# Kernel tuning notes

Measured on AMD Instinct MI355X. Metric: run time of the kernel, lower is better.

The kernel has to match this reference:

```python
import jax, jax.numpy as jnp
import numpy as np

B, C, H, W = 64, 3, 224, 224
DEPTH = 2
NUM_OPS = 14

def _lin(m, lo, hi):
    return lo + m * (hi - lo)

def _clip255(x):
    return jnp.clip(x, 0.0, 255.0)

def _affine_sample(img, a, b, c, d, e, f):
    # img: [C,H,W]; inverse map (x_out,y_out)->(a*x+b*y+c, d*x+e*y+f); bilinear, zero fill.
    ch, h, w = img.shape
    ys, xs = jnp.meshgrid(jnp.arange(h, dtype=img.dtype), jnp.arange(w, dtype=img.dtype), indexing='ij')
    sx = a * xs + b * ys + c
    sy = d * xs + e * ys + f
    x0 = jnp.floor(sx); y0 = jnp.floor(sy)
    wx = sx - x0; wy = sy - y0
    def gather(yi, xi):
        valid = (xi >= 0) & (xi <= w - 1) & (yi >= 0) & (yi <= h - 1)
        v = img[:, jnp.clip(yi, 0, h - 1).astype(jnp.int32), jnp.clip(xi, 0, w - 1).astype(jnp.int32)]
        return jnp.where(valid[None], v, 0.0)
    v00 = gather(y0, x0); v01 = gather(y0, x0 + 1)
    v10 = gather(y0 + 1, x0); v11 = gather(y0 + 1, x0 + 1)
    top = v00 * (1 - wx) + v01 * wx
    bot = v10 * (1 - wx) + v11 * wx
    return top * (1 - wy) + bot * wy

def _gray(img):
    lum = jnp.array([0.299, 0.587, 0.114], img.dtype)
    return jnp.einsum('chw,c->hw', img, lum)

def shear_x(img, m):
    v = _lin(m, -0.3, 0.3)
    return _affine_sample(img, 1.0, v, 0.0, 0.0, 1.0, 0.0)

def shear_y(img, m):
    v = _lin(m, -0.3, 0.3)
    return _affine_sample(img, 1.0, 0.0, 0.0, v, 1.0, 0.0)

def translate_x(img, m):
    v = _lin(m, -0.45, 0.45) * img.shape[2]
    return _affine_sample(img, 1.0, 0.0, v, 0.0, 1.0, 0.0)

def translate_y(img, m):
    v = _lin(m, -0.45, 0.45) * img.shape[1]
    return _affine_sample(img, 1.0, 0.0, 0.0, 0.0, 1.0, v)

def rotate(img, m):
    rad = _lin(m, -30.0, 30.0) * np.pi / 180.0
    cx = (img.shape[2] - 1) * 0.5
    cy = (img.shape[1] - 1) * 0.5
    cs, sn = jnp.cos(rad), jnp.sin(rad)
    c = cx - cs * cx - sn * cy
    f = cy + sn * cx - cs * cy
    return _affine_sample(img, cs, sn, c, -sn, cs, f)

def brightness(img, m):
    return _clip255(img * _lin(m, 0.1, 1.9))

def color(img, m):
    g = _gray(img)[None]
    return _clip255(g + _lin(m, 0.1, 1.9) * (img - g))

def sharpness(img, m):
    k = jnp.array([[1., 1., 1.], [1., 5., 1.], [1., 1., 1.]], img.dtype) / 13.0
    ch = img.shape[0]
    kern = jnp.tile(k[None, None], (ch, 1, 1, 1))  # [C,1,3,3] depthwise
    blur = jax.lax.conv_general_dilated(img[None], kern, (1, 1), 'SAME', feature_group_count=ch)[0]
    out = _clip255(blur + _lin(m, 0.1, 1.9) * (img - blur))
    # PIL keeps the 1-px border unchanged
    out = out.at[:, 0, :].set(img[:, 0, :]).at[:, -1, :].set(img[:, -1, :])
    out = out.at[:, :, 0].set(img[:, :, 0]).at[:, :, -1].set(img[:, :, -1])
    return out

def contrast(img, m):
    mu = jnp.mean(_gray(img))
    return _clip255(mu + _lin(m, 0.1, 1.9) * (img - mu))

def solarize(img, m):
    thr = _lin(m, 0.0, 256.0)
    return jnp.where(img < thr, img, 255.0 - img)

def posterize(img, m):
    nbits = jnp.round(_lin(m, 0.0, 4.0))  # bits removed -> keep 8-nbits
    q = 2.0 ** nbits
    return jnp.floor(img / q) * q

def equalize(img, m):
    def eq_ch(chan):
        v = jnp.clip(jnp.round(chan), 0, 255).astype(jnp.int32)
        hist = jnp.zeros(256, jnp.int32).at[v.ravel()].add(1)
        step = (jnp.sum(hist) - hist[255]) // 255
        cum = jnp.concatenate([jnp.zeros(1, jnp.int32), jnp.cumsum(hist)[:-1]])
        lut = jnp.where(step > 0,
                        jnp.clip((cum + step // 2) // jnp.maximum(step, 1), 0, 255),
                        jnp.arange(256))
        return lut[v].astype(chan.dtype)
    return jax.vmap(eq_ch)(img)

def autocontrast(img, m):
    lo = jnp.min(img, axis=(1, 2), keepdims=True)
    hi = jnp.max(img, axis=(1, 2), keepdims=True)
    scale = 255.0 / jnp.maximum(hi - lo, 1e-6)
    return jnp.where(hi > lo, _clip255((img - lo) * scale), img)

def identity(img, m):
    return img

BRANCHES = [shear_x, shear_y, translate_x, translate_y, rotate, brightness, color,
            sharpness, contrast, solarize, posterize, equalize, autocontrast, identity]

def setup_inputs() -> dict:
    key = jax.random.key(0)
    k1, k2, k3, k4, k5 = jax.random.split(key, 5)
    x = jax.random.uniform(k1, (B, C, H, W), jnp.float32)          # [0,1]; module scales by 255
    ra_deform = jax.random.uniform(k2, (DEPTH, B), jnp.float32)    # magnitudes in [0,1]
    op_idx = jax.random.randint(k3, (DEPTH, B), 0, NUM_OPS, jnp.int32)
    p = jax.random.uniform(k4, (DEPTH, B), jnp.float32, 0.2, 0.8)  # p_min_t..p_max_t
    apply_mask = jax.random.uniform(k5, (DEPTH, B), jnp.float32) < p
    return {"x": x, "ra_deform": ra_deform, "op_idx": op_idx, "apply_mask": apply_mask}

def reference(x, ra_deform, op_idx, apply_mask):
    x = x * jnp.where(jnp.max(x) <= 1.0, 255.0, 1.0)
    x = x.astype(jnp.float32)
    def apply_one(img, j, m, ap):
        out = jax.lax.switch(j, BRANCHES, img, m)
        return jnp.where(ap, out, img)
    for i in range(DEPTH):  # small fixed depth
        x = jax.vmap(apply_one)(x, op_idx[i], ra_deform[i], apply_mask[i])
    return jnp.clip(x / 255.0, 0.0, 1.0)
```

## Files before the change

kernel.cpp:

```cpp
#include <hip/hip_runtime.h>

#define WID 224
#define HGT 224
#define HWp 50176
#define CHW 150528
#define NB  64
#define NSL 2048
#define SCH 1568
#define NT  9408
#define TPI 147
#define TPC 49

#define OFF_MAXB   0
#define OFF_HIST1  256
#define OFF_PSUM0  49408
#define OFF_PMIN0  51456
#define OFF_PMAX0  57600
#define OFF_PHIST0 63744
#define OFF_PSUM1  3209472
#define OFF_PMIN1  3218880
#define OFF_PMAX1  3228288
#define OFF_INTER  3237696

__device__ __forceinline__ float clip255(float v){ return fminf(fmaxf(v, 0.f), 255.f); }

__device__ __forceinline__ float blk_reduce(float v, float* red, int tid, int op){
    red[tid] = v; __syncthreads();
    for (int s = 128; s > 0; s >>= 1){
        if (tid < s){
            float a = red[tid], b = red[tid+s];
            red[tid] = (op==0) ? a+b : (op==1 ? fminf(a,b) : fmaxf(a,b));
        }
        __syncthreads();
    }
    float r = red[0]; __syncthreads();
    return r;
}

__device__ __forceinline__ float samp(const float* __restrict__ pl, float yi, float xi, float scl){
    if (xi < 0.f || xi > (float)(WID-1) || yi < 0.f || yi > (float)(HGT-1)) return 0.f;
    return pl[(int)yi * WID + (int)xi] * scl;
}

__device__ __forceinline__ void lut_from_hist(const int* shh, float* slut, int tid){
    int step = (HWp - shh[255]) / 255;
    int cum = 0;
    for (int k = 0; k < tid; k++) cum += shh[k];
    int l = (step > 0) ? min(max((cum + (step >> 1)) / step, 0), 255) : tid;
    slut[tid] = (float)l;
}

__device__ __forceinline__ void apply_body(const float* __restrict__ img,
                                           int c, int p,
                                           int j, int ap, float m, float scl,
                                           float mu, float lo, float hi,
                                           const float* lut,
                                           float o[4])
{
    int y = p / WID;
    int x = p - y*WID;
    const float* pl = img + c*HWp;
    float4 v4 = *(const float4*)(pl + p);
    float iv[4] = {v4.x*scl, v4.y*scl, v4.z*scl, v4.w*scl};

    if (!ap) {
        #pragma unroll
        for (int k = 0; k < 4; k++) o[k] = iv[k];
        return;
    }
    switch (j){
    case 0: case 1: case 2: case 3: case 4: {
        float a = 1.f, bb = 0.f, cc = 0.f, dd = 0.f, ee = 1.f, ff = 0.f;
        if (j == 0)      bb = -0.3f + 0.6f*m;
        else if (j == 1) dd = -0.3f + 0.6f*m;
        else if (j == 2) cc = (-0.45f + 0.9f*m) * (float)WID;
        else if (j == 3) ff = (-0.45f + 0.9f*m) * (float)HGT;
        else {
            float deg = -30.f + 60.f*m;
            float rad = deg * (float)(3.14159265358979323846/180.0);
            float cs = cosf(rad), sn = sinf(rad);
            float cx = (WID-1)*0.5f, cy = (HGT-1)*0.5f;
            a = cs; bb = sn; dd = -sn; ee = cs;
            cc = cx - cs*cx - sn*cy;
            ff = cy + sn*cx - cs*cy;
        }
        float yf = (float)y;
        #pragma unroll
        for (int k = 0; k < 4; k++){
            float xf = (float)(x + k);
            float sx = a*xf + bb*yf + cc;
            float sy = dd*xf + ee*yf + ff;
            float x0f = floorf(sx), y0f = floorf(sy);
            float wx = sx - x0f, wy = sy - y0f;
            float v00 = samp(pl, y0f,     x0f,     scl);
            float v01 = samp(pl, y0f,     x0f+1.f, scl);
            float v10 = samp(pl, y0f+1.f, x0f,     scl);
            float v11 = samp(pl, y0f+1.f, x0f+1.f, scl);
            float top = v00*(1.f-wx) + v01*wx;
            float bot = v10*(1.f-wx) + v11*wx;
            o[k] = top*(1.f-wy) + bot*wy;
        }
        break; }
    case 5: {
        float f = 0.1f + 1.8f*m;
        #pragma unroll
        for (int k = 0; k < 4; k++) o[k] = clip255(iv[k]*f);
        break; }
    case 6: {
        float4 r4 = *(const float4*)(img + p);
        float4 g4 = *(const float4*)(img + HWp + p);
        float4 b4 = *(const float4*)(img + 2*HWp + p);
        float rr[4] = {r4.x*scl, r4.y*scl, r4.z*scl, r4.w*scl};
        float gg[4] = {g4.x*scl, g4.y*scl, g4.z*scl, g4.w*scl};
        float bl[4] = {b4.x*scl, b4.y*scl, b4.z*scl, b4.w*scl};
        float f = 0.1f + 1.8f*m;
        #pragma unroll
        for (int k = 0; k < 4; k++){
            float g = 0.299f*rr[k] + 0.587f*gg[k] + 0.114f*bl[k];
            o[k] = clip255(g + f*(iv[k] - g));
        }
        break; }
    case 7: {
        float f = 0.1f + 1.8f*m;
        #pragma unroll
        for (int k = 0; k < 4; k++){
            int xx = x + k;
            if (y == 0 || y == HGT-1 || xx == 0 || xx == WID-1) o[k] = iv[k];
            else {
                int q = p + k;
                float s8 = pl[q-WID-1] + pl[q-WID] + pl[q-WID+1]
                         + pl[q-1]     + pl[q+1]
                         + pl[q+WID-1] + pl[q+WID] + pl[q+WID+1];
                float blur = (s8*scl + 5.f*iv[k]) * (1.f/13.f);
                o[k] = clip255(blur + f*(iv[k] - blur));
            }
        }
        break; }
    case 8: {
        float f = 0.1f + 1.8f*m;
        #pragma unroll
        for (int k = 0; k < 4; k++) o[k] = clip255(mu + f*(iv[k] - mu));
        break; }
    case 9: {
        float thr = 256.f*m;
        #pragma unroll
        for (int k = 0; k < 4; k++) o[k] = (iv[k] < thr) ? iv[k] : 255.f - iv[k];
        break; }
    case 10: {
        float q = exp2f(rintf(4.f*m));
        #pragma unroll
        for (int k = 0; k < 4; k++) o[k] = floorf(iv[k]/q)*q;
        break; }
    case 11: {
        #pragma unroll
        for (int k = 0; k < 4; k++){
            int ivi = min(max((int)rintf(iv[k]), 0), 255);
            o[k] = lut[ivi];
        }
        break; }
    case 12: {
        float sc = 255.f / fmaxf(hi - lo, 1e-6f);
        #pragma unroll
        for (int k = 0; k < 4; k++)
            o[k] = (hi > lo) ? clip255((iv[k] - lo) * sc) : iv[k];
        break; }
    default:
        #pragma unroll
        for (int k = 0; k < 4; k++) o[k] = iv[k];
        break;
    }
}

__global__ void k1_stats(const float* __restrict__ x, const int* __restrict__ op,
                         const int* __restrict__ mask, float* __restrict__ wsf)
{
    __shared__ float red[256];
    __shared__ int sh[1536];
    int* ints = (int*)wsf;
    float* psum0 = wsf + OFF_PSUM0;
    float* pmin0 = wsf + OFF_PMIN0;
    float* pmax0 = wsf + OFF_PMAX0;
    int* phist0 = (int*)wsf + OFF_PHIST0;
    int* hist1  = (int*)wsf + OFF_HIST1;

    int blk = blockIdx.x, tid = threadIdx.x;
    if (tid < 24) hist1[blk*24 + tid] = 0;

    int b = blk >> 5, s = blk & 31;
    int j = op[b], ap = mask[b];
    bool needSum  = ap && (j == 8);
    bool needMM   = ap && (j == 12);
    bool needHist = ap && (j == 11);
    const float* img = x + (size_t)b * CHW;
    int p0 = s * SCH;
    const float GW[3] = {0.299f, 0.587f, 0.114f};

    float mx = 0.f, gs = 0.f;
    for (int c = 0; c < 3; c++){
        const float* pl = img + c*HWp + p0;
        float lo = 3.4e38f, hi = 0.f, cs = 0.f;
        for (int p = tid*4; p < SCH; p += 1024){
            float4 v = *(const float4*)(pl + p);
            float m4 = fmaxf(fmaxf(v.x, v.y), fmaxf(v.z, v.w));
            mx = fmaxf(mx, m4);
            if (needMM){ hi = fmaxf(hi, m4); lo = fminf(lo, fminf(fminf(v.x,v.y), fminf(v.z,v.w))); }
            if (needSum) cs += (v.x + v.y) + (v.z + v.w);
        }
        if (needSum) gs += GW[c] * cs;
        if (needMM){
            float l = blk_reduce(lo, red, tid, 1);
            if (!tid) pmin0[blk*3 + c] = l;
            float h = blk_reduce(hi, red, tid, 2);
            if (!tid) pmax0[blk*3 + c] = h;
        }
    }
    float bm = blk_reduce(mx, red, tid, 2);
    if (!tid) atomicMax(&ints[OFF_MAXB], __float_as_int(bm));
    if (needSum){
        float t = blk_reduce(gs, red, tid, 0);
        if (!tid) psum0[blk] = t;
    }
    if (needHist){
        for (int i = tid; i < 1536; i += 256) sh[i] = 0;
        __syncthreads();
        for (int c = 0; c < 3; c++){
            const float* pl = img + c*HWp + p0;
            for (int p = tid; p < SCH; p += 256){
                float v = pl[p];
                atomicAdd(&sh[c*256 + min(max((int)rintf(v), 0), 255)], 1);
                atomicAdd(&sh[768 + c*256 + min(max((int)rintf(v*255.f), 0), 255)], 1);
            }
        }
        __syncthreads();
        for (int i = tid; i < 1536; i += 256) phist0[blk*1536 + i] = sh[i];
    }
}

__global__ void k2_apply0(const float* __restrict__ x, const float* __restrict__ ra,
                          const int* __restrict__ op, const int* __restrict__ mask,
                          float* __restrict__ wsf)
{
    __shared__ float red[256];
    __shared__ int   shh[256];
    __shared__ float slut[256];
    const int* ints = (const int*)wsf;
    const float* psum0 = wsf + OFF_PSUM0;
    const float* pmin0 = wsf + OFF_PMIN0;
    const float* pmax0 = wsf + OFF_PMAX0;
    const int* phist0 = (const int*)wsf + OFF_PHIST0;
    int* hist1 = (int*)wsf + OFF_HIST1;
    float* psum1 = wsf + OFF_PSUM1;
    float* pmin1 = wsf + OFF_PMIN1;
    float* pmax1 = wsf + OFF_PMAX1;
    float* inter = wsf + OFF_INTER;

    int t = blockIdx.x, tid = threadIdx.x;
    int b = t / TPI;
    int r = t - b*TPI;
    int c = r / TPC;
    int p = (r - c*TPC)*1024 + tid*4;

    float scl = (__int_as_float(ints[OFF_MAXB]) <= 1.0f) ? 255.f : 1.f;
    int j = op[b], ap = mask[b];
    float m = ra[b];

    float mu = 0.f, lo = 0.f, hi = 0.f;
    const float* lut = nullptr;
    if (ap){
        if (j == 8){
            float v = (tid < 32) ? psum0[b*32 + tid] : 0.f;
            mu = blk_reduce(v, red, tid, 0) * scl * (1.f/(float)HWp);
        } else if (j == 12){
            float v  = (tid < 32) ? pmin0[(b*32 + tid)*3 + c] : 3.4e38f;
            lo = blk_reduce(v, red, tid, 1) * scl;
            float v2 = (tid < 32) ? pmax0[(b*32 + tid)*3 + c] : 0.f;
            hi = blk_reduce(v2, red, tid, 2) * scl;
        } else if (j == 11){
            int d = (scl == 255.f) ? 1 : 0;
            const int* ph = phist0 + d*768 + c*256 + tid;
            int sum = 0;
            #pragma unroll 8
            for (int s = 0; s < 32; s++) sum += ph[(b*32 + s)*1536];
            shh[tid] = sum;
            __syncthreads();
            lut_from_hist(shh, slut, tid);
            __syncthreads();
            lut = slut;
        }
    }

    float o[4];
    apply_body(x + (size_t)b*CHW, c, p, j, ap, m, scl, mu, lo, hi, lut, o);
    float4 w = {o[0], o[1], o[2], o[3]};
    *(float4*)(inter + (size_t)b*CHW + c*HWp + p) = w;

    int j1 = op[NB + b], ap1 = mask[NB + b];
    if (ap1 && (j1 == 8 || j1 == 11 || j1 == 12)){
        const float GW[3] = {0.299f, 0.587f, 0.114f};
        if (j1 == 8){
            float s4 = (o[0] + o[1]) + (o[2] + o[3]);
            float tot = blk_reduce(s4, red, tid, 0);
            if (!tid) psum1[t] = tot * GW[c];
        } else if (j1 == 12){
            float l4 = fminf(fminf(o[0],o[1]), fminf(o[2],o[3]));
            float h4 = fmaxf(fmaxf(o[0],o[1]), fmaxf(o[2],o[3]));
            float l = blk_reduce(l4, red, tid, 1);
            if (!tid) pmin1[t] = l;
            float h = blk_reduce(h4, red, tid, 2);
            if (!tid) pmax1[t] = h;
        } else {
            __syncthreads();
            shh[tid] = 0;
            __syncthreads();
            #pragma unroll
            for (int k = 0; k < 4; k++)
                atomicAdd(&shh[min(max((int)rintf(o[k]), 0), 255)], 1);
            __syncthreads();
            int v = shh[tid];
            if (v) atomicAdd(&hist1[b*768 + c*256 + tid], v);
        }
    }
}

__global__ void k3_apply1(const float* __restrict__ ra, const int* __restrict__ op,
                          const int* __restrict__ mask, float* __restrict__ out,
                          float* __restrict__ wsf)
{
    __shared__ float red[256];
    __shared__ int   shh[256];
    __shared__ float slut[256];
    const int* hist1 = (const int*)wsf + OFF_HIST1;
    const float* psum1 = wsf + OFF_PSUM1;
    const float* pmin1 = wsf + OFF_PMIN1;
    const float* pmax1 = wsf + OFF_PMAX1;
    const float* inter = wsf + OFF_INTER;

    int t = blockIdx.x, tid = threadIdx.x;
    int b = t / TPI;
    int r = t - b*TPI;
    int c = r / TPC;
    int p = (r - c*TPC)*1024 + tid*4;

    int j = op[NB + b], ap = mask[NB + b];
    float m = ra[NB + b];

    float mu = 0.f, lo = 0.f, hi = 0.f;
    const float* lut = nullptr;
    if (ap){
        if (j == 8){
            float v = (tid < TPI) ? psum1[b*TPI + tid] : 0.f;
            mu = blk_reduce(v, red, tid, 0) * (1.f/(float)HWp);
        } else if (j == 12){
            float v  = (tid < TPC) ? pmin1[b*TPI + c*TPC + tid] : 3.4e38f;
            lo = blk_reduce(v, red, tid, 1);
            float v2 = (tid < TPC) ? pmax1[b*TPI + c*TPC + tid] : 0.f;
            hi = blk_reduce(v2, red, tid, 2);
        } else if (j == 11){
            shh[tid] = hist1[b*768 + c*256 + tid];
            __syncthreads();
            lut_from_hist(shh, slut, tid);
            __syncthreads();
            lut = slut;
        }
    }

    float o[4];
    apply_body(inter + (size_t)b*CHW, c, p, j, ap, m, 1.f, mu, lo, hi, lut, o);
    float4 w;
    w.x = fminf(fmaxf(o[0]*(1.f/255.f), 0.f), 1.f);
    w.y = fminf(fmaxf(o[1]*(1.f/255.f), 0.f), 1.f);
    w.z = fminf(fmaxf(o[2]*(1.f/255.f), 0.f), 1.f);
    w.w = fminf(fmaxf(o[3]*(1.f/255.f), 0.f), 1.f);
    *(float4*)(out + (size_t)b*CHW + c*HWp + p) = w;
}

extern "C" void kernel_launch(void* const* d_in, const int* in_sizes, int n_in,
                              void* d_out, int out_size, void* d_ws, size_t ws_size,
                              hipStream_t stream) {
    const float* x    = (const float*)d_in[0];
    const float* ra   = (const float*)d_in[1];
    const int*   op   = (const int*)d_in[2];
    const int*   mask = (const int*)d_in[3];
    float* out = (float*)d_out;
    float* wsf = (float*)d_ws;

    k1_stats <<<NSL, 256, 0, stream>>>(x, op, mask, wsf);
    k2_apply0<<<NT,  256, 0, stream>>>(x, ra, op, mask, wsf);
    k3_apply1<<<NT,  256, 0, stream>>>(ra, op, mask, out, wsf);
}
```

Baseline: 149.6 us.

## Use wavefront shuffle reductions, parallel LUT scan, and XCD-aware block remapping

Block reductions now use 64-lane shuffles, with a four-entry shared-memory combine replacing the tree over 256 shared slots. Second-stage statistics are written per wavefront rather than per block, which removes the block-wide sync in the apply0 epilogue; workspace offsets grow to hold them. The serial per-thread cumulative histogram sum in the equalize LUT becomes a Hillis-Steele parallel prefix scan. Block indices are permuted so that consecutive tiles of one image are spread across the eight XCDs. The aim is fewer barriers and less serialized work, at the cost of more partials to reduce in k3 and a remap whose cache effect is uncertain.

```diff
diff --git a/kernel.cpp b/kernel.cpp
--- a/kernel.cpp
+++ b/kernel.cpp
@@ -18,36 +18,53 @@
 #define OFF_PMAX0  57600
 #define OFF_PHIST0 63744
 #define OFF_PSUM1  3209472
-#define OFF_PMIN1  3218880
-#define OFF_PMAX1  3228288
-#define OFF_INTER  3237696
+#define OFF_PMIN1  3247104
+#define OFF_PMAX1  3284736
+#define OFF_INTER  3322368
 
 __device__ __forceinline__ float clip255(float v){ return fminf(fmaxf(v, 0.f), 255.f); }
 
+__device__ __forceinline__ float wred(float v, int op){
+    #pragma unroll
+    for (int o = 32; o > 0; o >>= 1){
+        float u = __shfl_down(v, o);
+        v = (op==0) ? v+u : (op==1 ? fminf(v,u) : fmaxf(v,u));
+    }
+    return v;
+}
+
 __device__ __forceinline__ float blk_reduce(float v, float* red, int tid, int op){
-    red[tid] = v; __syncthreads();
-    for (int s = 128; s > 0; s >>= 1){
-        if (tid < s){
-            float a = red[tid], b = red[tid+s];
-            red[tid] = (op==0) ? a+b : (op==1 ? fminf(a,b) : fmaxf(a,b));
-        }
+    float w = wred(v, op);
+    if ((tid & 63) == 0) red[tid >> 6] = w;
+    __syncthreads();
+    float a = red[0], b = red[1], c = red[2], d = red[3];
+    float r = (op==0) ? (a+b)+(c+d) : (op==1 ? fminf(fminf(a,b),fminf(c,d)) : fmaxf(fmaxf(a,b),fmaxf(c,d)));
+    __syncthreads();
+    return r;
+}
+
+__device__ __forceinline__ const float* lut_scan(int hv, int* shh, float* slut, int tid, int* h255){
+    if (tid == 255) *h255 = hv;
+    shh[tid] = hv;
+    __syncthreads();
+    #pragma unroll
+    for (int off = 1; off < 256; off <<= 1){
+        int v = (tid >= off) ? shh[tid-off] : 0;
         __syncthreads();
-    }
-    float r = red[0]; __syncthreads();
-    return r;
+        shh[tid] += v;
+        __syncthreads();
+    }
+    int cum = shh[tid] - hv;
+    int step = (HWp - *h255) / 255;
+    int l = (step > 0) ? min(max((cum + (step >> 1)) / step, 0), 255) : tid;
+    slut[tid] = (float)l;
+    __syncthreads();
+    return slut;
 }
 
 __device__ __forceinline__ float samp(const float* __restrict__ pl, float yi, float xi, float scl){
     if (xi < 0.f || xi > (float)(WID-1) || yi < 0.f || yi > (float)(HGT-1)) return 0.f;
     return pl[(int)yi * WID + (int)xi] * scl;
-}
-
-__device__ __forceinline__ void lut_from_hist(const int* shh, float* slut, int tid){
-    int step = (HWp - shh[255]) / 255;
-    int cum = 0;
-    for (int k = 0; k < tid; k++) cum += shh[k];
-    int l = (step > 0) ? min(max((cum + (step >> 1)) / step, 0), 255) : tid;
-    slut[tid] = (float)l;
 }
 
 __device__ __forceinline__ void apply_body(const float* __restrict__ img,
@@ -174,7 +191,7 @@
 __global__ void k1_stats(const float* __restrict__ x, const int* __restrict__ op,
                          const int* __restrict__ mask, float* __restrict__ wsf)
 {
-    __shared__ float red[256];
+    __shared__ float red[4];
     __shared__ int sh[1536];
     int* ints = (int*)wsf;
     float* psum0 = wsf + OFF_PSUM0;
@@ -183,7 +200,8 @@
     int* phist0 = (int*)wsf + OFF_PHIST0;
     int* hist1  = (int*)wsf + OFF_HIST1;
 
-    int blk = blockIdx.x, tid = threadIdx.x;
+    int bid = blockIdx.x, tid = threadIdx.x;
+    int blk = ((bid & 7) << 8) + (bid >> 3);
     if (tid < 24) hist1[blk*24 + tid] = 0;
 
     int b = blk >> 5, s = blk & 31;
@@ -240,9 +258,10 @@
                           const int* __restrict__ op, const int* __restrict__ mask,
                           float* __restrict__ wsf)
 {
-    __shared__ float red[256];
+    __shared__ float red[4];
     __shared__ int   shh[256];
     __shared__ float slut[256];
+    __shared__ int   h255;
     const int* ints = (const int*)wsf;
     const float* psum0 = wsf + OFF_PSUM0;
     const float* pmin0 = wsf + OFF_PMIN0;
@@ -254,7 +273,8 @@
     float* pmax1 = wsf + OFF_PMAX1;
     float* inter = wsf + OFF_INTER;
 
-    int t = blockIdx.x, tid = threadIdx.x;
+    int bid = blockIdx.x, tid = threadIdx.x;
+    int t = ((bid & 7) * 1176) + (bid >> 3);
     int b = t / TPI;
     int r = t - b*TPI;
     int c = r / TPC;
@@ -281,11 +301,7 @@
             int sum = 0;
             #pragma unroll 8
             for (int s = 0; s < 32; s++) sum += ph[(b*32 + s)*1536];
-            shh[tid] = sum;
-            __syncthreads();
-            lut_from_hist(shh, slut, tid);
-            __syncthreads();
-            lut = slut;
+            lut = lut_scan(sum, shh, slut, tid, &h255);
         }
     }
 
@@ -297,17 +313,17 @@
     int j1 = op[NB + b], ap1 = mask[NB + b];
     if (ap1 && (j1 == 8 || j1 == 11 || j1 == 12)){
         const float GW[3] = {0.299f, 0.587f, 0.114f};
+        int wv = tid >> 6;
         if (j1 == 8){
             float s4 = (o[0] + o[1]) + (o[2] + o[3]);
-            float tot = blk_reduce(s4, red, tid, 0);
-            if (!tid) psum1[t] = tot * GW[c];
+            float ws = wred(s4, 0);
+            if ((tid & 63) == 0) psum1[t*4 + wv] = ws * GW[c];
         } else if (j1 == 12){
             float l4 = fminf(fminf(o[0],o[1]), fminf(o[2],o[3]));
             float h4 = fmaxf(fmaxf(o[0],o[1]), fmaxf(o[2],o[3]));
-            float l = blk_reduce(l4, red, tid, 1);
-            if (!tid) pmin1[t] = l;
-            float h = blk_reduce(h4, red, tid, 2);
-            if (!tid) pmax1[t] = h;
+            float wl = wred(l4, 1);
+            float wh = wred(h4, 2);
+            if ((tid & 63) == 0){ pmin1[t*4 + wv] = wl; pmax1[t*4 + wv] = wh; }
         } else {
             __syncthreads();
             shh[tid] = 0;
@@ -326,16 +342,18 @@
                           const int* __restrict__ mask, float* __restrict__ out,
                           float* __restrict__ wsf)
 {
-    __shared__ float red[256];
+    __shared__ float red[4];
     __shared__ int   shh[256];
     __shared__ float slut[256];
+    __shared__ int   h255;
     const int* hist1 = (const int*)wsf + OFF_HIST1;
     const float* psum1 = wsf + OFF_PSUM1;
     const float* pmin1 = wsf + OFF_PMIN1;
     const float* pmax1 = wsf + OFF_PMAX1;
     const float* inter = wsf + OFF_INTER;
 
-    int t = blockIdx.x, tid = threadIdx.x;
+    int bid = blockIdx.x, tid = threadIdx.x;
+    int t = ((bid & 7) * 1176) + (bid >> 3);
     int b = t / TPI;
     int r = t - b*TPI;
     int c = r / TPC;
@@ -348,19 +366,16 @@
     const float* lut = nullptr;
     if (ap){
         if (j == 8){
-            float v = (tid < TPI) ? psum1[b*TPI + tid] : 0.f;
+            float v = 0.f;
+            for (int i = tid; i < TPI*4; i += 256) v += psum1[b*TPI*4 + i];
             mu = blk_reduce(v, red, tid, 0) * (1.f/(float)HWp);
         } else if (j == 12){
-            float v  = (tid < TPC) ? pmin1[b*TPI + c*TPC + tid] : 3.4e38f;
+            float v  = (tid < TPC*4) ? pmin1[(b*TPI + c*TPC)*4 + tid] : 3.4e38f;
             lo = blk_reduce(v, red, tid, 1);
-            float v2 = (tid < TPC) ? pmax1[b*TPI + c*TPC + tid] : 0.f;
+            float v2 = (tid < TPC*4) ? pmax1[(b*TPI + c*TPC)*4 + tid] : 0.f;
             hi = blk_reduce(v2, red, tid, 2);
         } else if (j == 11){
-            shh[tid] = hist1[b*768 + c*256 + tid];
-            __syncthreads();
-            lut_from_hist(shh, slut, tid);
-            __syncthreads();
-            lut = slut;
+            lut = lut_scan(hist1[b*768 + c*256 + tid], shh, slut, tid, &h255);
         }
     }
 
```

After: 154.8 us. 3.5% more time.
